# Optimization experiments

Hardware: AMD Instinct MI355X
Metric: run time of the kernel (lower is better)

The kernel has to match this reference:

```python
import jax, jax.numpy as jnp
import numpy as np
from jax import lax


def _conv1(y, w):
    # y: (B, C) channel vector; w: (3,) Conv1d kernel (cross-correlation, pad=1, no bias)
    yp = jnp.pad(y, ((0, 0), (1, 1)))
    return w[0] * yp[:, :-2] + w[1] * yp[:, 1:-1] + w[2] * yp[:, 2:]


def _scale_branch(xs, dw_w, dw_b, ca_w, ra_w, gate_w, gate_b):
    # xs: (B, C, h, w) one scale of the multi-scale token map
    B, C = xs.shape[0], xs.shape[1]
    xs = lax.conv_general_dilated(
        xs, dw_w, (1, 1), 'SAME', feature_group_count=C,
        dimension_numbers=('NCHW', 'OIHW', 'NCHW')) + dw_b[None, :, None, None]
    avg = xs.mean(axis=(2, 3))          # (B, C) == AdaptiveAvgPool2d(1)
    mx = xs.max(axis=(2, 3))            # (B, C) == AdaptiveMaxPool2d(1)
    gw = jax.nn.softmax(avg @ gate_w + gate_b, axis=1)  # (B, 2) gating over experts
    pooled = avg + mx
    ca_s = jax.nn.sigmoid(_conv1(pooled, ca_w))          # CA channel gate
    ra_s = 1.0 - jax.nn.sigmoid(_conv1(pooled, ra_w))    # RA reverse gate
    # blend the two SE-style experts per channel, then broadcast-multiply
    scale = gw[:, 0:1] * ca_s + gw[:, 1:2] * ra_s        # (B, C)
    out = xs * scale[:, :, None, None]
    return out.reshape(B, C, -1).transpose(0, 2, 1)      # (B, h*w, C)


def setup_inputs() -> dict:
    key = jax.random.key(0)
    ks = jax.random.split(key, 12)
    B, N, Cin, Ch = 8, 5376, 384, 768
    s = lambda k, shape, fan: jax.random.normal(k, shape, jnp.float32) * (1.0 / np.sqrt(fan))
    return {
        'x': jax.random.normal(ks[0], (B, N, Cin), jnp.float32),
        'fc1_w': s(ks[1], (Cin, Ch), Cin),
        'fc1_b': jnp.zeros((Ch,), jnp.float32),
        'dw_w': s(ks[2], (Ch, 1, 3, 3), 9),
        'dw_b': jnp.zeros((Ch,), jnp.float32),
        'ca_w': s(ks[3], (3,), 3),
        'ra_w': s(ks[4], (3,), 3),
        'gate_w': s(ks[5], (Ch, 2), Ch),
        'gate_b': jnp.zeros((2,), jnp.float32),
        'fc2_w': s(ks[6], (Ch, Cin), Ch),
        'fc2_b': jnp.zeros((Cin,), jnp.float32),
        'H': 32,
        'W': 32,
    }


def reference(x, fc1_w, fc1_b, dw_w, dw_b, ca_w, ra_w, gate_w, gate_b, fc2_w, fc2_b, H, W):
    B, N, _ = x.shape
    C = fc1_w.shape[1]
    h = x @ fc1_w + fc1_b                     # fc1: (B, N, C)
    n = N // 21
    to_map = lambda seg, hh, ww: seg.transpose(0, 2, 1).reshape(B, C, hh, ww)
    x1 = to_map(h[:, :16 * n], 2 * H, 2 * W)
    x2 = to_map(h[:, 16 * n:20 * n], H, W)
    x3 = to_map(h[:, 20 * n:], H // 2, W // 2)
    parts = [_scale_branch(xi, dw_w, dw_b, ca_w, ra_w, gate_w, gate_b)
             for xi in (x1, x2, x3)]
    h = jnp.concatenate(parts, axis=1)        # (B, N, C)
    h = jax.nn.gelu(h, approximate=False)     # torch nn.GELU default = exact erf
    return h @ fc2_w + fc2_b
```

## Files before the change

kernel.cpp:

```cpp
#include <hip/hip_runtime.h>
#include <math.h>

#define B_   8
#define NTOK 5376
#define CIN  384
#define CH   768
#define M_   (B_*NTOK)

typedef unsigned short u16;
typedef unsigned int   u32;

using bf16x8 = __attribute__((ext_vector_type(8))) short;
using bf16x4 = __attribute__((ext_vector_type(4))) short;
using f32x4  = __attribute__((ext_vector_type(4))) float;

__device__ __forceinline__ u16 f2bf(float f) {
    union { float f; u32 u; } v; v.f = f;
    u32 r = v.u + 0x7fffu + ((v.u >> 16) & 1u);
    return (u16)(r >> 16);
}
__device__ __forceinline__ float bf2f(u16 u) {
    union { u32 u; float f; } v; v.u = ((u32)u) << 16;
    return v.f;
}
__device__ __forceinline__ u32 fkey(float f) {
    union { float f; u32 u; } v; v.f = f;
    return (v.u & 0x80000000u) ? ~v.u : (v.u | 0x80000000u);
}
__device__ __forceinline__ float fkeyinv(u32 k) {
    union { u32 u; float f; } v;
    v.u = (k & 0x80000000u) ? (k ^ 0x80000000u) : ~k;
    return v.f;
}

__global__ void k_cvt_x(const float* __restrict__ x, u16* __restrict__ xb, int n8) {
    int i = blockIdx.x * blockDim.x + threadIdx.x;
    if (i >= n8) return;
    float4 a = ((const float4*)x)[2 * i];
    float4 b = ((const float4*)x)[2 * i + 1];
    bf16x8 o;
    o[0] = (short)f2bf(a.x); o[1] = (short)f2bf(a.y);
    o[2] = (short)f2bf(a.z); o[3] = (short)f2bf(a.w);
    o[4] = (short)f2bf(b.x); o[5] = (short)f2bf(b.y);
    o[6] = (short)f2bf(b.z); o[7] = (short)f2bf(b.w);
    ((bf16x8*)xb)[i] = o;
}

__global__ void k_cvt_wT(const float* __restrict__ w, u16* __restrict__ wT, int K, int N) {
    int i = blockIdx.x * blockDim.x + threadIdx.x;
    if (i >= N * K) return;
    int n = i / K, k = i % K;
    wT[i] = f2bf(w[k * N + n]);
}

#define BM 128
#define BN 128
#define BK 64

template<bool OUT_BF16>
__launch_bounds__(256)
__global__ void gemm_bf16_kernel(const u16* __restrict__ A, const u16* __restrict__ Bt,
                                 const float* __restrict__ bias, void* __restrict__ Cout,
                                 int M, int N, int K) {
    __shared__ __align__(16) u16 sA[BM * BK];
    __shared__ __align__(16) u16 sB[BN * BK];
    const int mt = blockIdx.x, nt = blockIdx.y;
    const int tid = threadIdx.x;
    const int wave = tid >> 6, lane = tid & 63;
    const int wm = wave >> 1, wn = wave & 1;
    const int row0 = mt * BM, col0 = nt * BN;
    const int lr = lane & 15, lk = lane >> 4;

    f32x4 acc[4][4];
#pragma unroll
    for (int m = 0; m < 4; m++)
#pragma unroll
        for (int n = 0; n < 4; n++) acc[m][n] = (f32x4){0.f, 0.f, 0.f, 0.f};

    const int KT = K / BK;
    for (int kt = 0; kt < KT; ++kt) {
        const int k0 = kt * BK;
#pragma unroll
        for (int it = 0; it < 4; ++it) {
            int g  = it * 256 + tid;
            int r  = g >> 3;
            int ks = g & 7;
            const u16* gA = A + (size_t)(row0 + r) * K + k0 + ks * 8;
            const u16* gB = Bt + (size_t)(col0 + r) * K + k0 + ks * 8;
            u16* lA = sA + (size_t)(it * 256 + wave * 64) * 8;
            u16* lB = sB + (size_t)(it * 256 + wave * 64) * 8;
            __builtin_amdgcn_global_load_lds(
                (const __attribute__((address_space(1))) u32*)(const void*)gA,
                (__attribute__((address_space(3))) u32*)(void*)lA, 16, 0, 0);
            __builtin_amdgcn_global_load_lds(
                (const __attribute__((address_space(1))) u32*)(const void*)gB,
                (__attribute__((address_space(3))) u32*)(void*)lB, 16, 0, 0);
        }
        __syncthreads();
#pragma unroll
        for (int kk = 0; kk < 2; ++kk) {
            bf16x8 af[4], bfr[4];
#pragma unroll
            for (int m = 0; m < 4; m++)
                af[m] = *(const bf16x8*)&sA[(wm * 64 + m * 16 + lr) * BK + kk * 32 + lk * 8];
#pragma unroll
            for (int n = 0; n < 4; n++)
                bfr[n] = *(const bf16x8*)&sB[(wn * 64 + n * 16 + lr) * BK + kk * 32 + lk * 8];
#pragma unroll
            for (int m = 0; m < 4; m++)
#pragma unroll
                for (int n = 0; n < 4; n++)
                    acc[m][n] = __builtin_amdgcn_mfma_f32_16x16x32_bf16(af[m], bfr[n], acc[m][n], 0, 0, 0);
        }
        __syncthreads();
    }

#pragma unroll
    for (int m = 0; m < 4; m++) {
#pragma unroll
        for (int n = 0; n < 4; n++) {
            int col = col0 + wn * 64 + n * 16 + lr;
            float bv = bias[col];
#pragma unroll
            for (int r = 0; r < 4; r++) {
                int row = row0 + wm * 64 + m * 16 + lk * 4 + r;
                float v = acc[m][n][r] + bv;
                if (OUT_BF16)
                    ((u16*)Cout)[(size_t)row * N + col] = f2bf(v);
                else
                    ((float*)Cout)[(size_t)row * N + col] = v;
            }
        }
    }
}

__launch_bounds__(192)
__global__ void k_conv(const u16* __restrict__ h, const float* __restrict__ dw_w,
                       const float* __restrict__ dw_b, u16* __restrict__ xs,
                       float* __restrict__ psum, u32* __restrict__ pmaxk) {
    const int tile = blockIdx.x, b = blockIdx.y;
    int s, xt, yt, tokbase, LW;
    if (tile < 64)      { s = 0; xt = tile & 7;  yt = tile >> 3; tokbase = 0;    LW = 6; }
    else if (tile < 80) { int u = tile - 64; s = 1; xt = u & 3; yt = u >> 2; tokbase = 4096; LW = 5; }
    else                { int u = tile - 80; s = 2; xt = u & 1; yt = u >> 1; tokbase = 5120; LW = 4; }
    const int W = 1 << LW, H = W;
    const int x0 = xt * 8, y0 = yt * 8;
    const int c0 = threadIdx.x * 4;

    float wv[9][4], dwb[4];
#pragma unroll
    for (int j = 0; j < 4; j++) {
        dwb[j] = dw_b[c0 + j];
#pragma unroll
        for (int t = 0; t < 9; t++) wv[t][j] = dw_w[(c0 + j) * 9 + t];
    }

    const size_t base = ((size_t)(b * NTOK + tokbase)) * CH + c0;
    const bf16x4 z4 = (bf16x4){0, 0, 0, 0};
    bool colv[10];
    int coloff[10];
#pragma unroll
    for (int j = 0; j < 10; j++) {
        int xx = x0 - 1 + j;
        colv[j] = (xx >= 0) && (xx < W);
        coloff[j] = xx * CH;
    }

    bf16x4 r[3][10];

#define LOADROW(slot, yrow) {                                                   \
        int yr_ = (yrow);                                                       \
        bool rv_ = ((unsigned)yr_ < (unsigned)H);                               \
        int rb_ = yr_ * W * CH;                                                 \
        _Pragma("unroll")                                                       \
        for (int j = 0; j < 10; j++)                                            \
            r[slot][j] = (rv_ && colv[j]) ? *(const bf16x4*)&h[base + rb_ + coloff[j]] : z4; \
    }

    LOADROW(0, y0 - 1);
    LOADROW(1, y0);

    float as[4] = {0.f, 0.f, 0.f, 0.f};
    float am[4] = {-3.4e38f, -3.4e38f, -3.4e38f, -3.4e38f};

#pragma unroll
    for (int yy = 0; yy < 8; ++yy) {
        const int sm1 = yy % 3, sc = (yy + 1) % 3, sp1 = (yy + 2) % 3;
        LOADROW(sp1, y0 + yy + 1);
        const int orow = (y0 + yy) * W * CH;
#pragma unroll
        for (int p = 0; p < 8; ++p) {
            float o[4];
#pragma unroll
            for (int j = 0; j < 4; j++) o[j] = dwb[j];
#pragma unroll
            for (int kx = 0; kx < 3; ++kx) {
                const int ci = p + kx;
#pragma unroll
                for (int j = 0; j < 4; j++) {
                    o[j] += wv[0 + kx][j] * bf2f((u16)r[sm1][ci][j]);
                    o[j] += wv[3 + kx][j] * bf2f((u16)r[sc ][ci][j]);
                    o[j] += wv[6 + kx][j] * bf2f((u16)r[sp1][ci][j]);
                }
            }
            bf16x4 ov;
#pragma unroll
            for (int j = 0; j < 4; j++) {
                ov[j] = (short)f2bf(o[j]);
                as[j] += o[j];
                am[j] = fmaxf(am[j], o[j]);
            }
            *(bf16x4*)&xs[base + orow + (x0 + p) * CH] = ov;
        }
    }
#undef LOADROW

#pragma unroll
    for (int j = 0; j < 4; j++) {
        atomicAdd(&psum[(s * 8 + b) * CH + c0 + j], as[j]);
        atomicMax(&pmaxk[(s * 8 + b) * CH + c0 + j], fkey(am[j]));
    }
}

__global__ void k_scale(const float* __restrict__ psum, const u32* __restrict__ pmaxk,
                        const float* __restrict__ gate_w, const float* __restrict__ gate_b,
                        const float* __restrict__ ca_w, const float* __restrict__ ra_w,
                        float* __restrict__ scale) {
    int s = blockIdx.x, b = blockIdx.y;
    int tid = threadIdx.x;
    float npos = (s == 0) ? 4096.f : (s == 1) ? 1024.f : 256.f;
    __shared__ float pooled[CH];
    __shared__ float rl[4][2];
    float l0 = 0.f, l1 = 0.f;
#pragma unroll
    for (int j = 0; j < 3; j++) {
        int c = j * 256 + tid;
        size_t idx = ((size_t)s * 8 + b) * CH + c;
        float avg = psum[idx] / npos;
        float mxv = fkeyinv(pmaxk[idx]);
        pooled[c] = avg + mxv;
        l0 += avg * gate_w[c * 2 + 0];
        l1 += avg * gate_w[c * 2 + 1];
    }
    for (int off = 32; off; off >>= 1) {
        l0 += __shfl_down(l0, off);
        l1 += __shfl_down(l1, off);
    }
    int wave = tid >> 6, lane = tid & 63;
    if (lane == 0) { rl[wave][0] = l0; rl[wave][1] = l1; }
    __syncthreads();
    float L0 = rl[0][0] + rl[1][0] + rl[2][0] + rl[3][0] + gate_b[0];
    float L1 = rl[0][1] + rl[1][1] + rl[2][1] + rl[3][1] + gate_b[1];
    float mxl = fmaxf(L0, L1);
    float e0 = expf(L0 - mxl), e1 = expf(L1 - mxl);
    float g0 = e0 / (e0 + e1), g1 = e1 / (e0 + e1);
    float cw0 = ca_w[0], cw1 = ca_w[1], cw2 = ca_w[2];
    float rw0 = ra_w[0], rw1 = ra_w[1], rw2 = ra_w[2];
#pragma unroll
    for (int j = 0; j < 3; j++) {
        int c = j * 256 + tid;
        float pm = (c > 0)      ? pooled[c - 1] : 0.f;
        float pc = pooled[c];
        float pp = (c < CH - 1) ? pooled[c + 1] : 0.f;
        float cas = 1.f / (1.f + expf(-(cw0 * pm + cw1 * pc + cw2 * pp)));
        float ras = 1.f - 1.f / (1.f + expf(-(rw0 * pm + rw1 * pc + rw2 * pp)));
        scale[((size_t)s * 8 + b) * CH + c] = g0 * cas + g1 * ras;
    }
}

#define NG (M_ * (CH / 8))
__global__ void k_apply(u16* __restrict__ xs, const float* __restrict__ scale) {
    for (int gi = blockIdx.x * blockDim.x + threadIdx.x; gi < NG;
         gi += gridDim.x * blockDim.x) {
        int c8 = gi % 96;
        int tl = gi / 96;
        int t = tl % NTOK, b = tl / NTOK;
        int s = (t < 4096) ? 0 : (t < 5120 ? 1 : 2);
        const float4* sp = (const float4*)&scale[((size_t)(s * 8 + b)) * CH + c8 * 8];
        float4 sc0 = sp[0], sc1 = sp[1];
        float scv[8] = {sc0.x, sc0.y, sc0.z, sc0.w, sc1.x, sc1.y, sc1.z, sc1.w};
        bf16x8 v = *(const bf16x8*)&xs[(size_t)gi * 8];
        bf16x8 o;
#pragma unroll
        for (int j = 0; j < 8; j++) {
            float f = bf2f((u16)v[j]) * scv[j];
            float gl = 0.5f * f * (1.f + erff(f * 0.70710678118654752f));
            o[j] = (short)f2bf(gl);
        }
        *(bf16x8*)&xs[(size_t)gi * 8] = o;
    }
}

extern "C" void kernel_launch(void* const* d_in, const int* in_sizes, int n_in,
                              void* d_out, int out_size, void* d_ws, size_t ws_size,
                              hipStream_t stream) {
    const float* x      = (const float*)d_in[0];
    const float* fc1_w  = (const float*)d_in[1];
    const float* fc1_b  = (const float*)d_in[2];
    const float* dw_w   = (const float*)d_in[3];
    const float* dw_b   = (const float*)d_in[4];
    const float* ca_w   = (const float*)d_in[5];
    const float* ra_w   = (const float*)d_in[6];
    const float* gate_w = (const float*)d_in[7];
    const float* gate_b = (const float*)d_in[8];
    const float* fc2_w  = (const float*)d_in[9];
    const float* fc2_b  = (const float*)d_in[10];

    char* ws = (char*)d_ws;
    u16*  xb    = (u16*)(ws);
    u16*  hb    = (u16*)(ws + 33030144);
    u16*  xs    = (u16*)(ws + 99090432);
    u16*  w1T   = (u16*)(ws + 165150720);
    u16*  w2T   = (u16*)(ws + 165740544);
    float* psum = (float*)(ws + 166330368);
    u32*  pmaxk = (u32*)(ws + 166404096);
    float* scale= (float*)(ws + 166477824);

    hipMemsetAsync((void*)psum, 0, 147456, stream);

    k_cvt_x<<<(M_ * CIN / 8 + 255) / 256, 256, 0, stream>>>(x, xb, M_ * CIN / 8);
    k_cvt_wT<<<(CIN * CH + 255) / 256, 256, 0, stream>>>(fc1_w, w1T, CIN, CH);
    k_cvt_wT<<<(CIN * CH + 255) / 256, 256, 0, stream>>>(fc2_w, w2T, CH, CIN);

    gemm_bf16_kernel<true><<<dim3(M_ / BM, CH / BN), 256, 0, stream>>>(
        xb, w1T, fc1_b, (void*)hb, M_, CH, CIN);

    k_conv<<<dim3(84, 8), 192, 0, stream>>>(hb, dw_w, dw_b, xs, psum, pmaxk);

    k_scale<<<dim3(3, 8), 256, 0, stream>>>(psum, pmaxk, gate_w, gate_b, ca_w, ra_w, scale);

    k_apply<<<4096, 256, 0, stream>>>(xs, scale);

    gemm_bf16_kernel<false><<<dim3(M_ / BM, CIN / BN), 256, 0, stream>>>(
        xs, w2T, fc2_b, d_out, M_, CIN, CH);
}
```

Before: 336.7 us.

## Fuse fp32 input conversion into fc1 GEMM and scale+GELU into fc2 A-load

Removes the separate x-to-bf16 conversion kernel by having the fc1 GEMM read fp32 x, convert, and store it into LDS. Removes the scale/GELU apply pass by applying the per-channel scale and exact GELU while loading A tiles in the fc2 GEMM. This drops two full-tensor read/write passes. The cost is that A is now loaded through registers instead of direct global-to-LDS loads, and GELU is recomputed once per N-tile (three times) in fc2. The depthwise conv also goes from 4 to 2 channels per thread with 384-thread blocks.

After: 413.2 us. 22.7% more time.

```diff
diff --git a/kernel.cpp b/kernel.cpp
--- a/kernel.cpp
+++ b/kernel.cpp
@@ -12,6 +12,7 @@
 
 using bf16x8 = __attribute__((ext_vector_type(8))) short;
 using bf16x4 = __attribute__((ext_vector_type(4))) short;
+using bf16x2 = __attribute__((ext_vector_type(2))) short;
 using f32x4  = __attribute__((ext_vector_type(4))) float;
 
 __device__ __forceinline__ u16 f2bf(float f) {
@@ -32,18 +33,8 @@
     v.u = (k & 0x80000000u) ? (k ^ 0x80000000u) : ~k;
     return v.f;
 }
-
-__global__ void k_cvt_x(const float* __restrict__ x, u16* __restrict__ xb, int n8) {
-    int i = blockIdx.x * blockDim.x + threadIdx.x;
-    if (i >= n8) return;
-    float4 a = ((const float4*)x)[2 * i];
-    float4 b = ((const float4*)x)[2 * i + 1];
-    bf16x8 o;
-    o[0] = (short)f2bf(a.x); o[1] = (short)f2bf(a.y);
-    o[2] = (short)f2bf(a.z); o[3] = (short)f2bf(a.w);
-    o[4] = (short)f2bf(b.x); o[5] = (short)f2bf(b.y);
-    o[6] = (short)f2bf(b.z); o[7] = (short)f2bf(b.w);
-    ((bf16x8*)xb)[i] = o;
+__device__ __forceinline__ float gelu_exact(float f) {
+    return 0.5f * f * (1.f + erff(f * 0.70710678118654752f));
 }
 
 __global__ void k_cvt_wT(const float* __restrict__ w, u16* __restrict__ wT, int K, int N) {
@@ -57,11 +48,11 @@
 #define BN 128
 #define BK 64
 
-template<bool OUT_BF16>
+template<int AM, bool OUT_BF16>
 __launch_bounds__(256)
-__global__ void gemm_bf16_kernel(const u16* __restrict__ A, const u16* __restrict__ Bt,
-                                 const float* __restrict__ bias, void* __restrict__ Cout,
-                                 int M, int N, int K) {
+__global__ void gemm_fused(const void* __restrict__ Asrc, const u16* __restrict__ Bt,
+                           const float* __restrict__ bias, const float* __restrict__ scale_all,
+                           void* __restrict__ Cout, int M, int N, int K) {
     __shared__ __align__(16) u16 sA[BM * BK];
     __shared__ __align__(16) u16 sB[BN * BK];
     const int mt = blockIdx.x, nt = blockIdx.y;
@@ -71,6 +62,14 @@
     const int row0 = mt * BM, col0 = nt * BN;
     const int lr = lane & 15, lk = lane >> 4;
 
+    const float* srow = scale_all;
+    if (AM == 1) {
+        int b  = row0 / NTOK;
+        int t0 = row0 - b * NTOK;
+        int s  = (t0 < 4096) ? 0 : (t0 < 5120 ? 1 : 2);
+        srow = scale_all + ((size_t)(s * 8 + b)) * CH;
+    }
+
     f32x4 acc[4][4];
 #pragma unroll
     for (int m = 0; m < 4; m++)
@@ -85,16 +84,39 @@
             int g  = it * 256 + tid;
             int r  = g >> 3;
             int ks = g & 7;
-            const u16* gA = A + (size_t)(row0 + r) * K + k0 + ks * 8;
             const u16* gB = Bt + (size_t)(col0 + r) * K + k0 + ks * 8;
-            u16* lA = sA + (size_t)(it * 256 + wave * 64) * 8;
             u16* lB = sB + (size_t)(it * 256 + wave * 64) * 8;
-            __builtin_amdgcn_global_load_lds(
-                (const __attribute__((address_space(1))) u32*)(const void*)gA,
-                (__attribute__((address_space(3))) u32*)(void*)lA, 16, 0, 0);
             __builtin_amdgcn_global_load_lds(
                 (const __attribute__((address_space(1))) u32*)(const void*)gB,
                 (__attribute__((address_space(3))) u32*)(void*)lB, 16, 0, 0);
+        }
+#pragma unroll
+        for (int it = 0; it < 4; ++it) {
+            int g  = it * 256 + tid;
+            int r  = g >> 3;
+            int ks = g & 7;
+            bf16x8 o;
+            if (AM == 0) {
+                const float* ga = (const float*)Asrc + (size_t)(row0 + r) * K + k0 + ks * 8;
+                float4 a0 = ((const float4*)ga)[0];
+                float4 a1 = ((const float4*)ga)[1];
+                o[0] = (short)f2bf(a0.x); o[1] = (short)f2bf(a0.y);
+                o[2] = (short)f2bf(a0.z); o[3] = (short)f2bf(a0.w);
+                o[4] = (short)f2bf(a1.x); o[5] = (short)f2bf(a1.y);
+                o[6] = (short)f2bf(a1.z); o[7] = (short)f2bf(a1.w);
+            } else {
+                const u16* ga = (const u16*)Asrc + (size_t)(row0 + r) * K + k0 + ks * 8;
+                bf16x8 v = *(const bf16x8*)ga;
+                const float4* sp = (const float4*)&srow[k0 + ks * 8];
+                float4 s0 = sp[0], s1 = sp[1];
+                float scv[8] = {s0.x, s0.y, s0.z, s0.w, s1.x, s1.y, s1.z, s1.w};
+#pragma unroll
+                for (int j = 0; j < 8; j++) {
+                    float f = bf2f((u16)v[j]) * scv[j];
+                    o[j] = (short)f2bf(gelu_exact(f));
+                }
+            }
+            *(bf16x8*)&sA[(size_t)g * 8] = o;
         }
         __syncthreads();
 #pragma unroll
@@ -134,7 +156,7 @@
     }
 }
 
-__launch_bounds__(192)
+__launch_bounds__(384)
 __global__ void k_conv(const u16* __restrict__ h, const float* __restrict__ dw_w,
                        const float* __restrict__ dw_b, u16* __restrict__ xs,
                        float* __restrict__ psum, u32* __restrict__ pmaxk) {
@@ -145,18 +167,18 @@
     else                { int u = tile - 80; s = 2; xt = u & 1; yt = u >> 1; tokbase = 5120; LW = 4; }
     const int W = 1 << LW, H = W;
     const int x0 = xt * 8, y0 = yt * 8;
-    const int c0 = threadIdx.x * 4;
-
-    float wv[9][4], dwb[4];
-#pragma unroll
-    for (int j = 0; j < 4; j++) {
+    const int c0 = threadIdx.x * 2;
+
+    float wv[9][2], dwb[2];
+#pragma unroll
+    for (int j = 0; j < 2; j++) {
         dwb[j] = dw_b[c0 + j];
 #pragma unroll
         for (int t = 0; t < 9; t++) wv[t][j] = dw_w[(c0 + j) * 9 + t];
     }
 
     const size_t base = ((size_t)(b * NTOK + tokbase)) * CH + c0;
-    const bf16x4 z4 = (bf16x4){0, 0, 0, 0};
+    const bf16x2 z2 = (bf16x2){0, 0};
     bool colv[10];
     int coloff[10];
 #pragma unroll
@@ -166,7 +188,7 @@
         coloff[j] = xx * CH;
     }
 
-    bf16x4 r[3][10];
+    bf16x2 r[3][10];
 
 #define LOADROW(slot, yrow) {                                                   \
         int yr_ = (yrow);                                                       \
@@ -174,14 +196,14 @@
         int rb_ = yr_ * W * CH;                                                 \
         _Pragma("unroll")                                                       \
         for (int j = 0; j < 10; j++)                                            \
-            r[slot][j] = (rv_ && colv[j]) ? *(const bf16x4*)&h[base + rb_ + coloff[j]] : z4; \
+            r[slot][j] = (rv_ && colv[j]) ? *(const bf16x2*)&h[base + rb_ + coloff[j]] : z2; \
     }
 
     LOADROW(0, y0 - 1);
     LOADROW(1, y0);
 
-    float as[4] = {0.f, 0.f, 0.f, 0.f};
-    float am[4] = {-3.4e38f, -3.4e38f, -3.4e38f, -3.4e38f};
+    float as[2] = {0.f, 0.f};
+    float am[2] = {-3.4e38f, -3.4e38f};
 
 #pragma unroll
     for (int yy = 0; yy < 8; ++yy) {
@@ -190,33 +212,33 @@
         const int orow = (y0 + yy) * W * CH;
 #pragma unroll
         for (int p = 0; p < 8; ++p) {
-            float o[4];
-#pragma unroll
-            for (int j = 0; j < 4; j++) o[j] = dwb[j];
+            float o[2];
+#pragma unroll
+            for (int j = 0; j < 2; j++) o[j] = dwb[j];
 #pragma unroll
             for (int kx = 0; kx < 3; ++kx) {
                 const int ci = p + kx;
 #pragma unroll
-                for (int j = 0; j < 4; j++) {
+                for (int j = 0; j < 2; j++) {
                     o[j] += wv[0 + kx][j] * bf2f((u16)r[sm1][ci][j]);
                     o[j] += wv[3 + kx][j] * bf2f((u16)r[sc ][ci][j]);
                     o[j] += wv[6 + kx][j] * bf2f((u16)r[sp1][ci][j]);
                 }
             }
-            bf16x4 ov;
-#pragma unroll
-            for (int j = 0; j < 4; j++) {
+            bf16x2 ov;
+#pragma unroll
+            for (int j = 0; j < 2; j++) {
                 ov[j] = (short)f2bf(o[j]);
                 as[j] += o[j];
                 am[j] = fmaxf(am[j], o[j]);
             }
-            *(bf16x4*)&xs[base + orow + (x0 + p) * CH] = ov;
+            *(bf16x2*)&xs[base + orow + (x0 + p) * CH] = ov;
         }
     }
 #undef LOADROW
 
 #pragma unroll
-    for (int j = 0; j < 4; j++) {
+    for (int j = 0; j < 2; j++) {
         atomicAdd(&psum[(s * 8 + b) * CH + c0 + j], as[j]);
         atomicMax(&pmaxk[(s * 8 + b) * CH + c0 + j], fkey(am[j]));
     }
@@ -265,29 +287,6 @@
         float cas = 1.f / (1.f + expf(-(cw0 * pm + cw1 * pc + cw2 * pp)));
         float ras = 1.f - 1.f / (1.f + expf(-(rw0 * pm + rw1 * pc + rw2 * pp)));
         scale[((size_t)s * 8 + b) * CH + c] = g0 * cas + g1 * ras;
-    }
-}
-
-#define NG (M_ * (CH / 8))
-__global__ void k_apply(u16* __restrict__ xs, const float* __restrict__ scale) {
-    for (int gi = blockIdx.x * blockDim.x + threadIdx.x; gi < NG;
-         gi += gridDim.x * blockDim.x) {
-        int c8 = gi % 96;
-        int tl = gi / 96;
-        int t = tl % NTOK, b = tl / NTOK;
-        int s = (t < 4096) ? 0 : (t < 5120 ? 1 : 2);
-        const float4* sp = (const float4*)&scale[((size_t)(s * 8 + b)) * CH + c8 * 8];
-        float4 sc0 = sp[0], sc1 = sp[1];
-        float scv[8] = {sc0.x, sc0.y, sc0.z, sc0.w, sc1.x, sc1.y, sc1.z, sc1.w};
-        bf16x8 v = *(const bf16x8*)&xs[(size_t)gi * 8];
-        bf16x8 o;
-#pragma unroll
-        for (int j = 0; j < 8; j++) {
-            float f = bf2f((u16)v[j]) * scv[j];
-            float gl = 0.5f * f * (1.f + erff(f * 0.70710678118654752f));
-            o[j] = (short)f2bf(gl);
-        }
-        *(bf16x8*)&xs[(size_t)gi * 8] = o;
     }
 }
 
@@ -307,30 +306,26 @@
     const float* fc2_b  = (const float*)d_in[10];
 
     char* ws = (char*)d_ws;
-    u16*  xb    = (u16*)(ws);
-    u16*  hb    = (u16*)(ws + 33030144);
-    u16*  xs    = (u16*)(ws + 99090432);
-    u16*  w1T   = (u16*)(ws + 165150720);
-    u16*  w2T   = (u16*)(ws + 165740544);
-    float* psum = (float*)(ws + 166330368);
-    u32*  pmaxk = (u32*)(ws + 166404096);
-    float* scale= (float*)(ws + 166477824);
+    u16*  hb    = (u16*)(ws);
+    u16*  xs    = (u16*)(ws + 66060288);
+    u16*  w1T   = (u16*)(ws + 132120576);
+    u16*  w2T   = (u16*)(ws + 132710400);
+    float* psum = (float*)(ws + 133300224);
+    u32*  pmaxk = (u32*)(ws + 133373952);
+    float* scale= (float*)(ws + 133447680);
 
     hipMemsetAsync((void*)psum, 0, 147456, stream);
 
-    k_cvt_x<<<(M_ * CIN / 8 + 255) / 256, 256, 0, stream>>>(x, xb, M_ * CIN / 8);
     k_cvt_wT<<<(CIN * CH + 255) / 256, 256, 0, stream>>>(fc1_w, w1T, CIN, CH);
     k_cvt_wT<<<(CIN * CH + 255) / 256, 256, 0, stream>>>(fc2_w, w2T, CH, CIN);
 
-    gemm_bf16_kernel<true><<<dim3(M_ / BM, CH / BN), 256, 0, stream>>>(
-        xb, w1T, fc1_b, (void*)hb, M_, CH, CIN);
-
-    k_conv<<<dim3(84, 8), 192, 0, stream>>>(hb, dw_w, dw_b, xs, psum, pmaxk);
+    gemm_fused<0, true><<<dim3(M_ / BM, CH / BN), 256, 0, stream>>>(
+        (const void*)x, w1T, fc1_b, nullptr, (void*)hb, M_, CH, CIN);
+
+    k_conv<<<dim3(84, 8), 384, 0, stream>>>(hb, dw_w, dw_b, xs, psum, pmaxk);
 
     k_scale<<<dim3(3, 8), 256, 0, stream>>>(psum, pmaxk, gate_w, gate_b, ca_w, ra_w, scale);
 
-    k_apply<<<4096, 256, 0, stream>>>(xs, scale);
-
-    gemm_bf16_kernel<false><<<dim3(M_ / BM, CIN / BN), 256, 0, stream>>>(
-        xs, w2T, fc2_b, d_out, M_, CIN, CH);
-}
+    gemm_fused<1, false><<<dim3(M_ / BM, CIN / BN), 256, 0, stream>>>(
+        (const void*)xs, w2T, fc2_b, scale, d_out, M_, CIN, CH);
+}
```
